# Performance work log

Hardware: AMD Instinct MI355X
Metric: run time of the kernel (lower is better)

The kernel has to match this reference:

```python
import jax, jax.numpy as jnp
import numpy as np

N_NODES = 10000
N_EDGES = 320000
N_REL = 460
N_BASES = 30
D = 200


def setup_inputs() -> dict:
    key = jax.random.key(0)
    k = jax.random.split(key, 8)
    x = jax.random.normal(k[0], (N_NODES, D), dtype=jnp.float32)
    edge_index = jax.random.randint(k[1], (2, N_EDGES), 0, N_NODES, dtype=jnp.int32)
    edge_type = jax.random.randint(k[2], (N_EDGES,), 0, N_REL, dtype=jnp.int32)
    # Xavier-uniform-like init scales
    w_bound = float(np.sqrt(6.0 / (D + D)))
    c_bound = float(np.sqrt(6.0 / (N_REL + N_BASES)))
    weight = jax.random.uniform(k[3], (N_BASES, D, D), minval=-w_bound, maxval=w_bound, dtype=jnp.float32)
    coeff = jax.random.uniform(k[4], (N_REL, N_BASES), minval=-c_bound, maxval=c_bound, dtype=jnp.float32)
    self_weight = jax.random.uniform(k[5], (D, D), minval=-w_bound, maxval=w_bound, dtype=jnp.float32)
    bias = jnp.zeros((D,), dtype=jnp.float32)
    return {
        "x": x,
        "weight": weight,
        "coeff": coeff,
        "self_weight": self_weight,
        "bias": bias,
        "edge_index": edge_index,
        "edge_type": edge_type,
        "num_nodes": N_NODES,
    }


def reference(x, weight, coeff, self_weight, bias, edge_index, edge_type, num_nodes):
    # RelationalGraphConv.forward:
    #   W_r = sum_b coeff[r, b] * V_b ; msg_e = x[src_e] @ W_{type_e}
    #   out[n] = (sum_{e: tgt_e = n} msg_e) / max(in_deg[n], 1) + x @ W_self + bias
    src = edge_index[0]
    tgt = edge_index[1]
    src_feats = x[src]                    # (E, d_in) gather
    edge_coeff = coeff[edge_type]         # (E, B) gather

    # msg_e = sum_b coeff[type_e, b] * (src_e @ V_b): scan over bases to avoid
    # materializing an (E, B, d_out) intermediate (same math as W_r = coeff @ V).
    def body(acc, inputs):
        Vb, cb = inputs                   # (d_in, d_out), (E,)
        return acc + (src_feats @ Vb) * cb[:, None], None

    msg0 = jnp.zeros((src.shape[0], weight.shape[2]), dtype=x.dtype)
    msg, _ = jax.lax.scan(body, msg0, (weight, edge_coeff.T))  # (E, d_out)

    out = jax.ops.segment_sum(msg, tgt, num_segments=num_nodes)              # (N, d_out)
    deg = jax.ops.segment_sum(jnp.ones_like(tgt, dtype=x.dtype), tgt, num_segments=num_nodes)
    out = out / jnp.clip(deg, 1.0)[:, None]
    out = out + x @ self_weight + bias
    return out
```

## Files before the change

### kernel.cpp

```cpp
#include <hip/hip_runtime.h>
#include <hip/hip_bf16.h>

#define N_NODES 10000
#define N_EDGES 320000
#define N_REL   460
#define N_BASES 30
#define DIM     200
#define KZ      6016
#define KT      6240
#define NSTEPS  195
#define NTILES  157
#define NFRAG   16
#define KSPLIT  6
#define PROWS   10048
#define TKELEM  2048

#define PREP_B  (NFRAG * NSTEPS * 512)
#define PREP_C  (N_REL * 16)
#define PREP_X  (N_NODES * 224)
#define S1_TOTAL (N_EDGES + PREP_B + PREP_C)
#define S2_TOTAL (N_EDGES + PREP_X)

using short8  = __attribute__((ext_vector_type(8))) short;
using floatx4 = __attribute__((ext_vector_type(4))) float;

__device__ __forceinline__ unsigned short f2bf(float f) {
    union { float f; unsigned u; } v; v.f = f;
    unsigned u = v.u;
    return (unsigned short)((u + 0x7fffu + ((u >> 16) & 1u)) >> 16);
}

__device__ __forceinline__ short8 pack8(const unsigned short* u) {
    union { unsigned short s[8]; short8 v; } p;
#pragma unroll
    for (int i = 0; i < 8; ++i) p.s[i] = u[i];
    return p.v;
}

__device__ __forceinline__ size_t asw_idx(int n, int c) {
    int t = n >> 6, sub = (n >> 4) & 3, rl = n & 15;
    int kk = c >> 5, w = c & 31;
    return (size_t)(t * NSTEPS + kk) * TKELEM + sub * 512 + rl * 32 + w;
}


__global__ void sort1_kernel(const int* __restrict__ tgt, int* __restrict__ deg,
                             const float* __restrict__ weight, const float* __restrict__ sw,
                             const float* __restrict__ coeff,
                             unsigned short* __restrict__ BSW, unsigned int* __restrict__ Cpair) {
    int idx = blockIdx.x * blockDim.x + threadIdx.x;
    if (idx < N_EDGES) {
        atomicAdd(&deg[tgt[idx]], 1);
        return;
    }
    idx -= N_EDGES;
    if (idx < PREP_B) {
        int f = idx / (NSTEPS * 512);
        int rem = idx - f * (NSTEPS * 512);
        int kk = rem / 512;
        int e = rem - kk * 512;
        int l = e >> 3, j = e & 7;
        int rB = f * 16 + (l & 15);
        int k  = kk * 32 + (l >> 4) * 8 + j;
        float v = 0.f;
        if (rB < DIM) {
            if (k < KZ) {
                if (k < N_BASES * DIM) {
                    int b = k / DIM, kc = k - b * DIM;
                    v = weight[(b * DIM + kc) * DIM + rB];
                }
            } else {
                int jj = k - KZ;
                if (jj < DIM) v = sw[jj * DIM + rB];
            }
        }
        BSW[idx] = f2bf(v);
        return;
    }
    idx -= PREP_B;
    if (idx < PREP_C) {
        int t = idx >> 4, m = idx & 15;
        unsigned lo = f2bf(coeff[t * N_BASES + m]);
        unsigned hi = (m + 16 < N_BASES) ? f2bf(coeff[t * N_BASES + m + 16]) : 0u;
        Cpair[idx] = lo | (hi << 16);
    }
}

__global__ __launch_bounds__(1024) void scan_kernel(const int* deg, int* starts,
                                                    int* cursor, float* dinv) {
    __shared__ int part[1024];
    int tid = threadIdx.x;
    const int PER = (N_NODES + 1023) / 1024;
    int base = tid * PER;
    int s = 0;
    for (int i = 0; i < PER; ++i) { int idx = base + i; if (idx < N_NODES) s += deg[idx]; }
    part[tid] = s; __syncthreads();
    for (int off = 1; off < 1024; off <<= 1) {
        int v = (tid >= off) ? part[tid - off] : 0;
        __syncthreads();
        part[tid] += v;
        __syncthreads();
    }
    int run = (tid > 0) ? part[tid - 1] : 0;
    for (int i = 0; i < PER; ++i) {
        int idx = base + i;
        if (idx < N_NODES) {
            int d = deg[idx];
            starts[idx] = run; cursor[idx] = run;
            dinv[idx] = 1.0f / (float)(d > 0 ? d : 1);
            run += d;
        }
    }
    if (tid == 1023) starts[N_NODES] = part[1023];
}


__global__ void sort2_kernel(const int* __restrict__ src, const int* __restrict__ tgt,
                             const int* __restrict__ etype, int* __restrict__ cursor,
                             int2* __restrict__ sedge,
                             const float* __restrict__ x, const int* __restrict__ deg,
                             unsigned short* __restrict__ Xbf, unsigned short* __restrict__ ASW) {
    int idx = blockIdx.x * blockDim.x + threadIdx.x;
    if (idx < N_EDGES) {
        int t = tgt[idx];
        int pos = atomicAdd(&cursor[t], 1);
        sedge[pos] = make_int2(src[idx], etype[idx]);
        return;
    }
    idx -= N_EDGES;
    if (idx < PREP_X) {
        int n = idx / 224, j = idx - n * 224;
        float v = (j < DIM) ? x[(size_t)n * DIM + j] : 0.f;
        if (j < DIM) Xbf[(size_t)n * DIM + j] = f2bf(v);
        int d = deg[n]; if (d < 1) d = 1;
        ASW[asw_idx(n, KZ + j)] = f2bf((float)d * v);
    }
}


__global__ __launch_bounds__(256) void agg_kernel(const unsigned short* __restrict__ Xbf,
                                                  const unsigned int* __restrict__ Cpair,
                                                  const int* __restrict__ starts,
                                                  const int2* __restrict__ sedge,
                                                  unsigned short* __restrict__ ASW) {
    __shared__ __align__(16) unsigned short zbuf[4][3232];
    int lane = threadIdx.x & 63;
    int wave = threadIdx.x >> 6;
    int n = blockIdx.x * 4 + wave;
    int ln = lane & 15, q = lane >> 4;

    floatx4 acc0[13], acc1[13];
#pragma unroll
    for (int f = 0; f < 13; ++f) {
        acc0[f] = (floatx4){0.f, 0.f, 0.f, 0.f};
        acc1[f] = acc0[f];
    }

    int e0 = starts[n], e1 = starts[n + 1];
    for (int kb = e0; kb < e1; kb += 32) {
        int eb = kb + 8 * q;
        unsigned short a0v[8], a1v[8];
        int srcs[8];
#pragma unroll
        for (int j = 0; j < 8; ++j) {
            int e = eb + j;
            int ec = (e < e1) ? e : (e1 - 1);
            int2 sd = sedge[ec];
            unsigned cp = (e < e1) ? Cpair[sd.y * 16 + ln] : 0u;
            a0v[j] = (unsigned short)(cp & 0xffffu);
            a1v[j] = (unsigned short)(cp >> 16);
            srcs[j] = sd.x;
        }
        short8 A0 = pack8(a0v), A1 = pack8(a1v);

        unsigned short bv[2][8];
#pragma unroll
        for (int j = 0; j < 8; ++j)
            bv[0][j] = Xbf[(size_t)srcs[j] * DIM + ln];
#pragma unroll
        for (int f = 0; f < 13; ++f) {
            int cur = f & 1, nxt = cur ^ 1;
            if (f < 12) {
#pragma unroll
                for (int j = 0; j < 8; ++j)
                    bv[nxt][j] = Xbf[(size_t)srcs[j] * DIM + (f + 1) * 16 + ln];
            }
            short8 B = pack8(bv[cur]);
            acc0[f] = __builtin_amdgcn_mfma_f32_16x16x32_bf16(A0, B, acc0[f], 0, 0, 0);
            acc1[f] = __builtin_amdgcn_mfma_f32_16x16x32_bf16(A1, B, acc1[f], 0, 0, 0);
        }
    }

    unsigned short* zb = zbuf[wave];
    int t = n >> 6, sub = (n >> 4) & 3, rl = n & 15;
    const uint4* zb4 = (const uint4*)zb;
    uint4* dst = (uint4*)ASW;
    size_t base_u4 = (size_t)t * NSTEPS * 256 + sub * 64 + rl * 4;

#pragma unroll
    for (int f = 0; f < 13; ++f) {
        int d = f * 16 + ln;
        if (d < DIM) {
#pragma unroll
            for (int i = 0; i < 4; ++i)
                zb[(q * 4 + i) * DIM + d] = f2bf(acc0[f][i]);
        }
    }
    for (int v = lane; v < 400; v += 64) {
        int kk = v >> 2, w8 = v & 3;
        dst[base_u4 + (size_t)kk * 256 + w8] = zb4[v];
    }

    if (lane < 16) zb[2800 + lane] = 0;
#pragma unroll
    for (int f = 0; f < 13; ++f) {
        int d = f * 16 + ln;
        if (d < DIM) {
#pragma unroll
            for (int i = 0; i < 4; ++i) {
                int b1 = 16 + q * 4 + i;
                if (b1 < N_BASES) zb[(b1 - 16) * DIM + d] = f2bf(acc1[f][i]);
            }
        }
    }
    for (int v = lane; v < 352; v += 64) {
        int kk = 100 + (v >> 2), w8 = v & 3;
        dst[base_u4 + (size_t)kk * 256 + w8] = zb4[v];
    }
}


__global__ __launch_bounds__(256) void gemm_kernel(const unsigned short* __restrict__ ASW,
                                                   const unsigned short* __restrict__ BSW,
                                                   float* __restrict__ part) {
    int tid = threadIdx.x;
    int lane = tid & 63, wave = tid >> 6;
    int tile = blockIdx.x, chunk = blockIdx.y;
    int ks = (chunk * NSTEPS) / KSPLIT;
    int ke = ((chunk + 1) * NSTEPS) / KSPLIT;
    int ln = lane & 15, q = lane >> 4;

    const unsigned short* pa = ASW + (size_t)tile * NSTEPS * TKELEM + ln * 32 + q * 8;
    const unsigned short* pb = BSW + (size_t)(wave * NSTEPS) * 512 + lane * 8;

    floatx4 acc[4][4];
#pragma unroll
    for (int i = 0; i < 4; ++i)
#pragma unroll
        for (int s = 0; s < 4; ++s) acc[i][s] = (floatx4){0.f, 0.f, 0.f, 0.f};

    short8 a0[4], b0[4], a1[4], b1[4];

    auto lda = [&](short8* dst, int k) {
#pragma unroll
        for (int s = 0; s < 4; ++s)
            dst[s] = *(const short8*)(pa + (size_t)k * TKELEM + s * 512);
    };
    auto ldb = [&](short8* dst, int k) {
#pragma unroll
        for (int i = 0; i < 4; ++i)
            dst[i] = *(const short8*)(pb + ((size_t)i * 4 * NSTEPS + k) * 512);
    };
    auto mfma16 = [&](short8* a, short8* b) {
#pragma unroll
        for (int i = 0; i < 4; ++i)
#pragma unroll
            for (int s = 0; s < 4; ++s)
                acc[i][s] = __builtin_amdgcn_mfma_f32_16x16x32_bf16(a[s], b[i], acc[i][s], 0, 0, 0);
    };

    lda(a0, ks); ldb(b0, ks);
    int k1 = (ks + 1 < ke) ? ks + 1 : ks;
    lda(a1, k1); ldb(b1, k1);

    int kk = ks;
    for (; kk + 2 < ke; kk += 2) {
        mfma16(a0, b0);
        lda(a0, kk + 2); ldb(b0, kk + 2);
        mfma16(a1, b1);
        int k3 = (kk + 3 < ke) ? kk + 3 : ke - 1;
        lda(a1, k3); ldb(b1, k3);
    }
    mfma16(a0, b0);
    if (kk + 1 < ke) mfma16(a1, b1);

    int row0 = tile * 64;
    float* pbase = part + ((size_t)chunk * PROWS + row0) * 208;
#pragma unroll
    for (int i = 0; i < 4; ++i) {
        int fg = wave + 4 * i;
        if (fg < 13) {
            int c = fg * 16 + ln;
#pragma unroll
            for (int s = 0; s < 4; ++s)
#pragma unroll
                for (int ii = 0; ii < 4; ++ii)
                    pbase[(s * 16 + q * 4 + ii) * 208 + c] = acc[i][s][ii];
        }
    }
}


__global__ __launch_bounds__(256) void reduce_kernel(const float* __restrict__ part,
                                                     const float* __restrict__ dinv,
                                                     const float* __restrict__ bias,
                                                     float* __restrict__ out) {
    int idx = blockIdx.x * blockDim.x + threadIdx.x;
    if (idx >= N_NODES * 50) return;
    int r = idx / 50, cq = idx - r * 50;
    float4 s = {0.f, 0.f, 0.f, 0.f};
#pragma unroll
    for (int c = 0; c < KSPLIT; ++c) {
        float4 v = *(const float4*)(part + ((size_t)c * PROWS + r) * 208 + cq * 4);
        s.x += v.x; s.y += v.y; s.z += v.z; s.w += v.w;
    }
    float dv = dinv[r];
    float4 b = *(const float4*)(bias + cq * 4);
    float4 o;
    o.x = s.x * dv + b.x; o.y = s.y * dv + b.y;
    o.z = s.z * dv + b.z; o.w = s.w * dv + b.w;
    *(float4*)(out + (size_t)r * DIM + cq * 4) = o;
}


extern "C" void kernel_launch(void* const* d_in, const int* in_sizes, int n_in,
                              void* d_out, int out_size, void* d_ws, size_t ws_size,
                              hipStream_t stream) {
    const float* x      = (const float*)d_in[0];
    const float* weight = (const float*)d_in[1];
    const float* coeff  = (const float*)d_in[2];
    const float* selfw  = (const float*)d_in[3];
    const float* bias   = (const float*)d_in[4];
    const int*   eidx   = (const int*)d_in[5];
    const int*   etype  = (const int*)d_in[6];
    const int* src = eidx;
    const int* tgt = eidx + N_EDGES;
    float* out = (float*)d_out;

    char* ws = (char*)d_ws;
    size_t off = 0;
    auto carve = [&](size_t bytes) {
        char* p = ws + off;
        off += (bytes + 255) & ~(size_t)255;
        return p;
    };
    unsigned short* ASW  = (unsigned short*)carve((size_t)NTILES * NSTEPS * TKELEM * 2);
    unsigned short* BSW  = (unsigned short*)carve((size_t)NFRAG * NSTEPS * 512 * 2);
    float* part   = (float*)carve((size_t)KSPLIT * PROWS * 208 * 4);
    unsigned short* Xbf  = (unsigned short*)carve((size_t)(N_NODES * DIM + 64) * 2);
    unsigned int*  Cpair = (unsigned int*)carve((size_t)N_REL * 16 * 4);
    int*   deg    = (int*)carve((size_t)N_NODES * 4);
    int*   starts = (int*)carve((size_t)(N_NODES + 1) * 4);
    int*   cursor = (int*)carve((size_t)N_NODES * 4);
    float* dinv   = (float*)carve((size_t)N_NODES * 4);
    int2*  sedge  = (int2*)carve((size_t)N_EDGES * 8);

    hipMemsetAsync(deg, 0, (size_t)N_NODES * 4, stream);

    sort1_kernel<<<(S1_TOTAL + 255) / 256, 256, 0, stream>>>(
        tgt, deg, weight, selfw, coeff, BSW, Cpair);

    scan_kernel<<<1, 1024, 0, stream>>>(deg, starts, cursor, dinv);

    sort2_kernel<<<(S2_TOTAL + 255) / 256, 256, 0, stream>>>(
        src, tgt, etype, cursor, sedge, x, deg, Xbf, ASW);

    agg_kernel<<<N_NODES / 4, 256, 0, stream>>>(Xbf, Cpair, starts, sedge, ASW);

    dim3 ggrid(NTILES, KSPLIT);
    gemm_kernel<<<ggrid, 256, 0, stream>>>(ASW, BSW, part);

    reduce_kernel<<<(N_NODES * 50 + 255) / 256, 256, 0, stream>>>(part, dinv, bias, out);
}
```

Measured before the change: 254.4 us.

## Stage A tiles through LDS with deep async global_load_lds pipeline in GEMM

Replaces direct register loads of the A operand with an 8-slot LDS ring buffer filled by async global_load_lds seven steps ahead, while B is double-buffered in registers. Explicit vmcnt waits and barriers sequence each step, and launch bounds now request 4 blocks per SM. The aim is to hide global load latency for the MFMA loop behind a deeper prefetch. In exchange it adds a per-step block barrier and 32KB of LDS per block, and depends on hand-counted vmcnt values being correct.

Result: no change. 253.1 us (-0.5%).

```diff
diff --git a/kernel.cpp b/kernel.cpp
--- a/kernel.cpp
+++ b/kernel.cpp
@@ -230,9 +230,39 @@
 }
 
 
-__global__ __launch_bounds__(256) void gemm_kernel(const unsigned short* __restrict__ ASW,
-                                                   const unsigned short* __restrict__ BSW,
-                                                   float* __restrict__ part) {
+#define GITER(VLIT, BU, BL, KK)                                                        \
+  {                                                                                    \
+    asm volatile("s_waitcnt vmcnt(" #VLIT ")" ::: "memory");                           \
+    __builtin_amdgcn_sched_barrier(0);                                                 \
+    asm volatile("s_barrier" ::: "memory");                                            \
+    const int kk_ = (KK);                                                              \
+    const int kld_ = (kk_ + 1 < ke) ? kk_ + 1 : ke - 1;                                \
+    BL[0] = *(const short8*)(pb + ((size_t)(0 * 4 * NSTEPS) + kld_) * 512);            \
+    BL[1] = *(const short8*)(pb + ((size_t)(1 * 4 * NSTEPS) + kld_) * 512);            \
+    BL[2] = *(const short8*)(pb + ((size_t)(2 * 4 * NSTEPS) + kld_) * 512);            \
+    BL[3] = *(const short8*)(pb + ((size_t)(3 * 4 * NSTEPS) + kld_) * 512);            \
+    const int kst_ = (kk_ + 7 < ke) ? kk_ + 7 : ke - 1;                                \
+    __builtin_amdgcn_global_load_lds(                                                  \
+        (const unsigned int*)(aswt + (size_t)kst_ * TKELEM + goff),                    \
+        (unsigned int*)(ldsw + ((kk_ + 7) & 7) * 2048), 16, 0, 0);                     \
+    const unsigned short* sp_ = alds + (kk_ & 7) * 2048 + pread8;                      \
+    short8 av0 = *(const short8*)(sp_);                                                \
+    short8 av1 = *(const short8*)(sp_ + 512);                                          \
+    short8 av2 = *(const short8*)(sp_ + 1024);                                         \
+    short8 av3 = *(const short8*)(sp_ + 1536);                                         \
+    _Pragma("unroll")                                                                  \
+    for (int i_ = 0; i_ < 4; ++i_) {                                                   \
+      acc[i_][0] = __builtin_amdgcn_mfma_f32_16x16x32_bf16(av0, BU[i_], acc[i_][0], 0, 0, 0); \
+      acc[i_][1] = __builtin_amdgcn_mfma_f32_16x16x32_bf16(av1, BU[i_], acc[i_][1], 0, 0, 0); \
+      acc[i_][2] = __builtin_amdgcn_mfma_f32_16x16x32_bf16(av2, BU[i_], acc[i_][2], 0, 0, 0); \
+      acc[i_][3] = __builtin_amdgcn_mfma_f32_16x16x32_bf16(av3, BU[i_], acc[i_][3], 0, 0, 0); \
+    }                                                                                  \
+  }
+
+__global__ __launch_bounds__(256, 4) void gemm_kernel(const unsigned short* __restrict__ ASW,
+                                                      const unsigned short* __restrict__ BSW,
+                                                      float* __restrict__ part) {
+    __shared__ __align__(16) unsigned short alds[8 * 2048];
     int tid = threadIdx.x;
     int lane = tid & 63, wave = tid >> 6;
     int tile = blockIdx.x, chunk = blockIdx.y;
@@ -240,49 +270,44 @@
     int ke = ((chunk + 1) * NSTEPS) / KSPLIT;
     int ln = lane & 15, q = lane >> 4;
 
-    const unsigned short* pa = ASW + (size_t)tile * NSTEPS * TKELEM + ln * 32 + q * 8;
+    const unsigned short* aswt = ASW + (size_t)tile * NSTEPS * TKELEM;
     const unsigned short* pb = BSW + (size_t)(wave * NSTEPS) * 512 + lane * 8;
 
+    int gsw = (tid & 0xE0) | ((tid & 7) << 2) | ((tid >> 3) & 3);
+    int goff = gsw * 8;
+    int pread8 = ((((ln >> 3) & 1) << 5) | (q << 3) | (ln & 7)) * 8;
+    unsigned short* ldsw = alds + wave * 512;
+
     floatx4 acc[4][4];
 #pragma unroll
     for (int i = 0; i < 4; ++i)
 #pragma unroll
         for (int s = 0; s < 4; ++s) acc[i][s] = (floatx4){0.f, 0.f, 0.f, 0.f};
 
-    short8 a0[4], b0[4], a1[4], b1[4];
-
-    auto lda = [&](short8* dst, int k) {
-#pragma unroll
-        for (int s = 0; s < 4; ++s)
-            dst[s] = *(const short8*)(pa + (size_t)k * TKELEM + s * 512);
-    };
-    auto ldb = [&](short8* dst, int k) {
-#pragma unroll
-        for (int i = 0; i < 4; ++i)
-            dst[i] = *(const short8*)(pb + ((size_t)i * 4 * NSTEPS + k) * 512);
-    };
-    auto mfma16 = [&](short8* a, short8* b) {
-#pragma unroll
-        for (int i = 0; i < 4; ++i)
-#pragma unroll
-            for (int s = 0; s < 4; ++s)
-                acc[i][s] = __builtin_amdgcn_mfma_f32_16x16x32_bf16(a[s], b[i], acc[i][s], 0, 0, 0);
-    };
-
-    lda(a0, ks); ldb(b0, ks);
-    int k1 = (ks + 1 < ke) ? ks + 1 : ks;
-    lda(a1, k1); ldb(b1, k1);
-
-    int kk = ks;
-    for (; kk + 2 < ke; kk += 2) {
-        mfma16(a0, b0);
-        lda(a0, kk + 2); ldb(b0, kk + 2);
-        mfma16(a1, b1);
-        int k3 = (kk + 3 < ke) ? kk + 3 : ke - 1;
-        lda(a1, k3); ldb(b1, k3);
-    }
-    mfma16(a0, b0);
-    if (kk + 1 < ke) mfma16(a1, b1);
+    short8 bA[4], bB[4];
+
+#pragma unroll
+    for (int i = 0; i < 4; ++i)
+        bA[i] = *(const short8*)(pb + ((size_t)(i * 4 * NSTEPS) + ks) * 512);
+#pragma unroll
+    for (int d = 0; d < 7; ++d)
+        __builtin_amdgcn_global_load_lds(
+            (const unsigned int*)(aswt + (size_t)(ks + d) * TKELEM + goff),
+            (unsigned int*)(ldsw + ((ks + d) & 7) * 2048), 16, 0, 0);
+
+    GITER(0,  bA, bB, ks + 0);
+    GITER(5,  bB, bA, ks + 1);
+    GITER(10, bA, bB, ks + 2);
+    GITER(15, bB, bA, ks + 3);
+    GITER(20, bA, bB, ks + 4);
+    GITER(25, bB, bA, ks + 5);
+
+    int kk = ks + 6;
+    for (; kk + 1 < ke; kk += 2) {
+        GITER(30, bA, bB, kk);
+        GITER(30, bB, bA, kk + 1);
+    }
+    if (kk < ke) { GITER(30, bA, bB, kk); }
 
     int row0 = tile * 64;
     float* pbase = part + ((size_t)chunk * PROWS + row0) * 208;
```
